# Kernel optimization log

Measured on AMD Instinct MI355X. Metric: run time of the kernel, lower is better.

## Reference

```python
import jax, jax.numpy as jnp
import numpy as np

INPUT_SIZE = 768
HIDDEN = [512, 256, 128]
LATENT = 32
NUM_LEVELS = 3
CODEBOOK_SIZE = 256
BATCH = 131072


def _init_linear(key, d_in, d_out):
    kw, kb = jax.random.split(key)
    lim = 1.0 / np.sqrt(d_in)
    W = jax.random.uniform(kw, (d_in, d_out), jnp.float32, -lim, lim)
    b = jax.random.uniform(kb, (d_out,), jnp.float32, -lim, lim)
    return W, b


def setup_inputs() -> dict:
    key = jax.random.key(0)
    keys = jax.random.split(key, 16)
    inp = {"x": jax.random.normal(keys[0], (BATCH, INPUT_SIZE), jnp.float32)}
    enc_dims = [INPUT_SIZE] + HIDDEN + [LATENT]          # 768->512->256->128->32
    dec_dims = [LATENT] + HIDDEN[::-1] + [INPUT_SIZE]     # 32->128->256->512->768
    for i in range(4):
        W, b = _init_linear(keys[1 + i], enc_dims[i], enc_dims[i + 1])
        inp[f"enc_W{i}"], inp[f"enc_b{i}"] = W, b
        W, b = _init_linear(keys[6 + i], dec_dims[i], dec_dims[i + 1])
        inp[f"dec_W{i}"], inp[f"dec_b{i}"] = W, b
    inp["codebooks"] = jax.random.normal(keys[12], (NUM_LEVELS, CODEBOOK_SIZE, LATENT), jnp.float32)
    return inp


def _mlp(x, Ws, bs):
    # Linear -> ReLU (-> Dropout p=0, identity) between layers, final layer linear.
    n = len(Ws)
    for i in range(n):
        x = x @ Ws[i] + bs[i]
        if i < n - 1:
            x = jax.nn.relu(x)
    return x


def _quantize(z, codebooks):
    # Residual vector quantization over NUM_LEVELS codebooks.
    L, K, D = codebooks.shape
    r = z
    idxs, rs, es = [], [], []
    for l in range(L):
        c = codebooks[l]                                  # [K, D]
        # squared-distance argmin (same argmin as cdist)
        d = jnp.sum(r * r, axis=-1, keepdims=True) - 2.0 * (r @ c.T) + jnp.sum(c * c, axis=-1)
        idx = jnp.argmin(d, axis=-1)                      # [B]
        e = c[idx]                                        # [B, D] gather
        idxs.append(idx)
        rs.append(r)
        es.append(e)
        r = r - e
    quantized = jnp.stack(idxs, axis=1)                   # [B, L] int codes
    r_stack = jnp.stack(rs, axis=1)                       # [B, L, D] residual inputs per level
    e_stack = jnp.stack(es, axis=1)                       # [B, L, D] selected embeddings
    sum_e = jnp.sum(e_stack, axis=1)                      # [B, D]
    # straight-through estimator
    z_hat = z + jax.lax.stop_gradient(sum_e - z)
    counts = jnp.sum(jax.nn.one_hot(quantized, K, dtype=jnp.float32), axis=0)  # [L, K] usage
    return quantized, r_stack, e_stack, z_hat, counts


def reference(x,
              enc_W0, enc_b0, enc_W1, enc_b1, enc_W2, enc_b2, enc_W3, enc_b3,
              dec_W0, dec_b0, dec_W1, dec_b1, dec_W2, dec_b2, dec_W3, dec_b3,
              codebooks):
    encoded = _mlp(x, [enc_W0, enc_W1, enc_W2, enc_W3], [enc_b0, enc_b1, enc_b2, enc_b3])
    quantized, r, e, z_hat, counts = _quantize(encoded, codebooks)
    decoded = _mlp(z_hat, [dec_W0, dec_W1, dec_W2, dec_W3], [dec_b0, dec_b1, dec_b2, dec_b3])
    return decoded, r, e, counts, quantized
```

## Files before the change

kernel.cpp:

```cpp
#include <hip/hip_runtime.h>
#include <hip/hip_bf16.h>
#include <cfloat>

#define B_TOTAL 131072
#define IN_DIM  768
#define NLEV    3
#define KCODE   256

typedef unsigned short u16;
typedef unsigned int   u32;
typedef __attribute__((ext_vector_type(8))) short bf16x8;
typedef __attribute__((ext_vector_type(4))) float f32x4;

#define GLOAD_LDS(g, l)                                                        \
    __builtin_amdgcn_global_load_lds(                                          \
        (const __attribute__((address_space(1))) u32*)(g),                     \
        (__attribute__((address_space(3))) u32*)(l), 16, 0, 0)

__device__ __forceinline__ u16 f2bf(float x) {
    union { __hip_bfloat16 h; u16 u; } c;
    c.h = __float2bfloat16(x);
    return c.u;
}
__device__ __forceinline__ float bf2f(u32 lo16) {
    union { u32 v; float f; } c;
    c.v = lo16 << 16;
    return c.f;
}
__device__ __forceinline__ u32 pack2(float a, float b) {
    return (u32)f2bf(a) | ((u32)f2bf(b) << 16);
}

template<int K, int N, bool AF32, bool RELU, bool OUTF32>
__global__ __launch_bounds__(256)
void gemm_mfma(const void* __restrict__ A_, const u16* __restrict__ Wt,
               const float* __restrict__ bias, void* __restrict__ C_)
{
    constexpr int NK  = K / 32;
    constexpr int NCB = N / 128;
    __shared__ u16 As[2][4096];
    __shared__ u16 Bs[2][4096];

    const int tid  = threadIdx.x;
    const int lane = tid & 63;
    const int wid  = tid >> 6;
    const int wrow = wid >> 1, wcol = wid & 1;

    const u32 nwg  = gridDim.x;
    const u32 orig = blockIdx.x;
    const u32 xcd = orig & 7u, q8 = nwg >> 3, r8 = nwg & 7u;
    const u32 wg = (xcd < r8 ? xcd * (q8 + 1) : r8 * (q8 + 1) + (xcd - r8) * q8)
                 + (orig >> 3);
    const int col0 = (int)(wg % NCB) * 128;
    const int row0 = (int)(wg / NCB) * 128;

    const u16*   Ab = (const u16*)A_;
    const float* Af = (const float*)A_;

    f32x4 acc[4][4];
    #pragma unroll
    for (int i = 0; i < 4; ++i)
        #pragma unroll
        for (int j = 0; j < 4; ++j) acc[i][j] = (f32x4){0.f, 0.f, 0.f, 0.f};

    auto stage_gld = [&](u16* dst, const u16* src ) {
        #pragma unroll
        for (int i = 0; i < 2; ++i) {
            const u32 o   = (u32)(i * 4096 + wid * 1024 + lane * 16);
            const u32 row = o >> 6;
            const u32 cb  = o & 63u;
            const u32 cbs = cb ^ ((row & 3u) << 4);
            const char* g = (const char*)(src + (size_t)row * K) + cbs;
            u16* l = dst + (i * 2048 + wid * 512);
            GLOAD_LDS(g, l);
        }
    };

    float4 fa[4];
    auto loadA_f32 = [&](int kt) {
        const int row = tid >> 1;
        const int ce0 = (tid & 1) * 16;
        const float* s = &Af[(size_t)(row0 + row) * K + kt * 32 + ce0];
        fa[0] = *(const float4*)(s + 0);
        fa[1] = *(const float4*)(s + 4);
        fa[2] = *(const float4*)(s + 8);
        fa[3] = *(const float4*)(s + 12);
    };
    auto writeA_f32 = [&](int buf) {
        const int row = tid >> 1;
        const int cb0 = (tid & 1) * 32;
        const int sw  = (row & 3) << 4;
        char* lb = (char*)&As[buf][0] + row * 64;
        *(uint4*)(lb + ((cb0 + 0) ^ sw)) = make_uint4(
            pack2(fa[0].x, fa[0].y), pack2(fa[0].z, fa[0].w),
            pack2(fa[1].x, fa[1].y), pack2(fa[1].z, fa[1].w));
        *(uint4*)(lb + ((cb0 + 16) ^ sw)) = make_uint4(
            pack2(fa[2].x, fa[2].y), pack2(fa[2].z, fa[2].w),
            pack2(fa[3].x, fa[3].y), pack2(fa[3].z, fa[3].w));
    };

    auto compute = [&](int buf) {
        const char* Ab8 = (const char*)&As[buf][0];
        const char* Bb8 = (const char*)&Bs[buf][0];
        const int kb = (lane >> 4) * 16;
        bf16x8 af[4], bf[4];
        #pragma unroll
        for (int mf = 0; mf < 4; ++mf) {
            const int r = wrow * 64 + mf * 16 + (lane & 15);
            af[mf] = *(const bf16x8*)(Ab8 + r * 64 + (kb ^ ((r & 3) << 4)));
        }
        #pragma unroll
        for (int nf = 0; nf < 4; ++nf) {
            const int r = wcol * 64 + nf * 16 + (lane & 15);
            bf[nf] = *(const bf16x8*)(Bb8 + r * 64 + (kb ^ ((r & 3) << 4)));
        }
        #pragma unroll
        for (int mf = 0; mf < 4; ++mf)
            #pragma unroll
            for (int nf = 0; nf < 4; ++nf)
                acc[mf][nf] = __builtin_amdgcn_mfma_f32_16x16x32_bf16(
                    af[mf], bf[nf], acc[mf][nf], 0, 0, 0);
    };

    if constexpr (AF32) loadA_f32(0);
    stage_gld(&Bs[0][0], Wt + (size_t)col0 * K);
    if constexpr (AF32) writeA_f32(0);
    else                stage_gld(&As[0][0], Ab + (size_t)row0 * K);
    __syncthreads();

    int cur = 0;
    #pragma unroll 1
    for (int kt = 0; kt < NK; ++kt) {
        const bool pref = (kt + 1 < NK);
        if (pref) {
            if constexpr (AF32) loadA_f32(kt + 1);
            stage_gld(&Bs[cur ^ 1][0], Wt + (size_t)col0 * K + (kt + 1) * 32);
            if constexpr (!AF32)
                stage_gld(&As[cur ^ 1][0], Ab + (size_t)row0 * K + (kt + 1) * 32);
        }
        compute(cur);
        if (pref) { if constexpr (AF32) writeA_f32(cur ^ 1); }
        __syncthreads();
        cur ^= 1;
    }

    #pragma unroll
    for (int nf = 0; nf < 4; ++nf) {
        const int col = col0 + wcol * 64 + nf * 16 + (lane & 15);
        const float bv = bias[col];
        #pragma unroll
        for (int mf = 0; mf < 4; ++mf) {
            const int rbase = row0 + wrow * 64 + mf * 16 + (lane >> 4) * 4;
            #pragma unroll
            for (int r = 0; r < 4; ++r) {
                float o = acc[mf][nf][r] + bv;
                if (RELU) o = fmaxf(o, 0.f);
                if constexpr (OUTF32)
                    ((float*)C_)[(size_t)(rbase + r) * N + col] = o;
                else
                    ((u16*)C_)[(size_t)(rbase + r) * N + col] = f2bf(o);
            }
        }
    }
}

template<int K, int N>
__global__ __launch_bounds__(256)
void wcvt(const float* __restrict__ W, u16* __restrict__ Wt)
{
    const int idx = blockIdx.x * 256 + threadIdx.x;
    const int k = idx / N, n = idx - k * N;
    Wt[(size_t)n * K + k] = f2bf(W[idx]);
}

__global__ __launch_bounds__(256)
void vq_kernel(const u16* __restrict__ h3, const float* __restrict__ eW3,
               const float* __restrict__ eb3, const float* __restrict__ cb,
               float* __restrict__ r_out, float* __restrict__ e_out,
               float* __restrict__ q_out, u16* __restrict__ se_ws,
               u32* __restrict__ ghist, size_t grow_base)
{
    __shared__ float W3[128 * 32];
    __shared__ float ebv[32];
    __shared__ float clds[256 * 36];
    __shared__ float cc2[256];
    __shared__ u32   lh[NLEV * KCODE];

    const int tid = threadIdx.x;
    const size_t lrow = (size_t)blockIdx.x * 256 + tid;
    const size_t grow = grow_base + lrow;

    for (int i = tid; i < 128 * 32; i += 256) W3[i] = eW3[i];
    if (tid < 32) ebv[tid] = eb3[tid];
    for (int i = tid; i < NLEV * KCODE; i += 256) lh[i] = 0;
    __syncthreads();

    float r[32];
    #pragma unroll
    for (int j = 0; j < 32; ++j) r[j] = ebv[j];
    {
        const u32* hrow = (const u32*)h3 + lrow * 64;
        #pragma unroll 2
        for (int k2 = 0; k2 < 64; ++k2) {
            const u32 v = hrow[k2];
            const float x0 = bf2f(v & 0xffffu), x1 = bf2f(v >> 16);
            const float* w0 = &W3[(2 * k2) * 32];
            const float* w1 = &W3[(2 * k2 + 1) * 32];
            #pragma unroll
            for (int j4 = 0; j4 < 8; ++j4) {
                const float4 a = *(const float4*)&w0[4 * j4];
                const float4 b = *(const float4*)&w1[4 * j4];
                r[4*j4+0] = fmaf(x1, b.x, fmaf(x0, a.x, r[4*j4+0]));
                r[4*j4+1] = fmaf(x1, b.y, fmaf(x0, a.y, r[4*j4+1]));
                r[4*j4+2] = fmaf(x1, b.z, fmaf(x0, a.z, r[4*j4+2]));
                r[4*j4+3] = fmaf(x1, b.w, fmaf(x0, a.w, r[4*j4+3]));
            }
        }
    }

    float z0[32];
    #pragma unroll
    for (int j = 0; j < 32; ++j) z0[j] = r[j];

    #pragma unroll 1
    for (int l = 0; l < NLEV; ++l) {
        __syncthreads();
        {
            const float* cl = cb + ((size_t)l * KCODE + tid) * 32;
            float s = 0.f;
            #pragma unroll
            for (int m = 0; m < 8; ++m) {
                const float4 v = *(const float4*)&cl[4 * m];
                *(float4*)&clds[tid * 36 + 4 * m] = v;
                s = fmaf(v.x, v.x, s); s = fmaf(v.y, v.y, s);
                s = fmaf(v.z, v.z, s); s = fmaf(v.w, v.w, s);
            }
            cc2[tid] = -0.5f * s;
        }
        __syncthreads();

        float best = -FLT_MAX;
        int   bidx = 0;
        #pragma unroll 1
        for (int k = 0; k < KCODE; ++k) {
            const float* ck = &clds[k * 36];
            float d0 = 0.f, d1 = 0.f, d2 = 0.f, d3 = 0.f;
            #pragma unroll
            for (int m = 0; m < 8; m += 4) {
                const float4 v0 = *(const float4*)&ck[4 * (m + 0)];
                const float4 v1 = *(const float4*)&ck[4 * (m + 1)];
                const float4 v2 = *(const float4*)&ck[4 * (m + 2)];
                const float4 v3 = *(const float4*)&ck[4 * (m + 3)];
                d0 = fmaf(r[4*m+0],  v0.x, d0); d0 = fmaf(r[4*m+1],  v0.y, d0);
                d0 = fmaf(r[4*m+2],  v0.z, d0); d0 = fmaf(r[4*m+3],  v0.w, d0);
                d1 = fmaf(r[4*m+4],  v1.x, d1); d1 = fmaf(r[4*m+5],  v1.y, d1);
                d1 = fmaf(r[4*m+6],  v1.z, d1); d1 = fmaf(r[4*m+7],  v1.w, d1);
                d2 = fmaf(r[4*m+8],  v2.x, d2); d2 = fmaf(r[4*m+9],  v2.y, d2);
                d2 = fmaf(r[4*m+10], v2.z, d2); d2 = fmaf(r[4*m+11], v2.w, d2);
                d3 = fmaf(r[4*m+12], v3.x, d3); d3 = fmaf(r[4*m+13], v3.y, d3);
                d3 = fmaf(r[4*m+14], v3.z, d3); d3 = fmaf(r[4*m+15], v3.w, d3);
            }
            const float s = ((d0 + d1) + (d2 + d3)) + cc2[k];
            if (s > best) { best = s; bidx = k; }
        }

        const size_t base = (grow * NLEV + l) * 32;
        const float* ce = &clds[bidx * 36];
        #pragma unroll
        for (int m = 0; m < 8; ++m) {
            const float4 ev = *(const float4*)&ce[4 * m];
            *(float4*)&r_out[base + 4 * m] =
                make_float4(r[4*m+0], r[4*m+1], r[4*m+2], r[4*m+3]);
            *(float4*)&e_out[base + 4 * m] = ev;
            r[4*m+0] -= ev.x; r[4*m+1] -= ev.y;
            r[4*m+2] -= ev.z; r[4*m+3] -= ev.w;
        }
        q_out[grow * NLEV + l] = (float)bidx;
        atomicAdd(&lh[l * KCODE + bidx], 1u);
    }

    u32* sed = (u32*)se_ws + lrow * 16;
    #pragma unroll
    for (int m = 0; m < 16; ++m)
        sed[m] = pack2(z0[2*m] - r[2*m], z0[2*m+1] - r[2*m+1]);

    __syncthreads();
    for (int i = tid; i < NLEV * KCODE; i += 256)
        if (lh[i]) atomicAdd(&ghist[i], lh[i]);
}

__global__ void zero_hist(u32* h) {
    if (threadIdx.x < NLEV * KCODE) h[threadIdx.x] = 0;
}
__global__ void counts_fin(const u32* __restrict__ g, float* __restrict__ o) {
    if (threadIdx.x < NLEV * KCODE) o[threadIdx.x] = (float)g[threadIdx.x];
}

__global__ __launch_bounds__(256)
void counts_k(const float* __restrict__ q, float* __restrict__ cnt)
{
    const int l = blockIdx.x >> 8;
    const int k = blockIdx.x & 255;
    const float pat = (float)k;
    int c = 0;
    for (int i = threadIdx.x; i < B_TOTAL; i += 256)
        c += (q[(size_t)i * NLEV + l] == pat) ? 1 : 0;
    __shared__ int red[256];
    red[threadIdx.x] = c;
    __syncthreads();
    for (int s = 128; s > 0; s >>= 1) {
        if (threadIdx.x < s) red[threadIdx.x] += red[threadIdx.x + s];
        __syncthreads();
    }
    if (threadIdx.x == 0)
        cnt[blockIdx.x] = (float)red[0];
}

template<int K, int N, bool RELU, bool AGLOBAL>
static __device__ __forceinline__
void layer16(const float* __restrict__ A, size_t grow0,
             const float* __restrict__ W, const float* __restrict__ bias,
             float* __restrict__ C)
{
    constexpr int QPT = N / 128;
    const int tr = threadIdx.x >> 5;
    const int tc = threadIdx.x & 31;
    float acc[2][QPT * 4];
    #pragma unroll
    for (int i = 0; i < 2; ++i)
        #pragma unroll
        for (int j = 0; j < QPT * 4; ++j) acc[i][j] = 0.f;
    #pragma unroll 2
    for (int k0 = 0; k0 < K; k0 += 4) {
        float4 av[2];
        #pragma unroll
        for (int i = 0; i < 2; ++i) {
            if (AGLOBAL)
                av[i] = *(const float4*)&A[(grow0 + tr * 2 + i) * (size_t)K + k0];
            else
                av[i] = *(const float4*)&A[(tr * 2 + i) * K + k0];
        }
        #pragma unroll
        for (int kk = 0; kk < 4; ++kk) {
            #pragma unroll
            for (int q = 0; q < QPT; ++q) {
                const float4 w4 = *(const float4*)&W[(size_t)(k0 + kk) * N + 4 * (tc + 32 * q)];
                #pragma unroll
                for (int i = 0; i < 2; ++i) {
                    const float a = ((const float*)&av[i])[kk];
                    acc[i][4*q+0] = fmaf(a, w4.x, acc[i][4*q+0]);
                    acc[i][4*q+1] = fmaf(a, w4.y, acc[i][4*q+1]);
                    acc[i][4*q+2] = fmaf(a, w4.z, acc[i][4*q+2]);
                    acc[i][4*q+3] = fmaf(a, w4.w, acc[i][4*q+3]);
                }
            }
        }
    }
    #pragma unroll
    for (int q = 0; q < QPT; ++q) {
        const float4 b4 = *(const float4*)&bias[4 * (tc + 32 * q)];
        #pragma unroll
        for (int i = 0; i < 2; ++i) {
            float4 o;
            o.x = acc[i][4*q+0] + b4.x; o.y = acc[i][4*q+1] + b4.y;
            o.z = acc[i][4*q+2] + b4.z; o.w = acc[i][4*q+3] + b4.w;
            if (RELU) {
                o.x = fmaxf(o.x, 0.f); o.y = fmaxf(o.y, 0.f);
                o.z = fmaxf(o.z, 0.f); o.w = fmaxf(o.w, 0.f);
            }
            *(float4*)&C[(tr * 2 + i) * N + 4 * (tc + 32 * q)] = o;
        }
    }
}

static __device__ __forceinline__
void layer_final16(const float* __restrict__ A, const float* __restrict__ W,
                   const float* __restrict__ bias, float* __restrict__ Cg, size_t grow0)
{
    constexpr int QPT = 6;
    const int tr = threadIdx.x >> 5;
    const int tc = threadIdx.x & 31;
    float acc[2][QPT * 4];
    #pragma unroll
    for (int i = 0; i < 2; ++i)
        #pragma unroll
        for (int j = 0; j < QPT * 4; ++j) acc[i][j] = 0.f;
    #pragma unroll 2
    for (int k0 = 0; k0 < 512; k0 += 4) {
        float4 av[2];
        #pragma unroll
        for (int i = 0; i < 2; ++i)
            av[i] = *(const float4*)&A[(tr * 2 + i) * 512 + k0];
        #pragma unroll
        for (int kk = 0; kk < 4; ++kk) {
            #pragma unroll
            for (int q = 0; q < QPT; ++q) {
                const float4 w4 = *(const float4*)&W[(size_t)(k0 + kk) * 768 + 4 * (tc + 32 * q)];
                #pragma unroll
                for (int i = 0; i < 2; ++i) {
                    const float a = ((const float*)&av[i])[kk];
                    acc[i][4*q+0] = fmaf(a, w4.x, acc[i][4*q+0]);
                    acc[i][4*q+1] = fmaf(a, w4.y, acc[i][4*q+1]);
                    acc[i][4*q+2] = fmaf(a, w4.z, acc[i][4*q+2]);
                    acc[i][4*q+3] = fmaf(a, w4.w, acc[i][4*q+3]);
                }
            }
        }
    }
    #pragma unroll
    for (int q = 0; q < QPT; ++q) {
        const float4 b4 = *(const float4*)&bias[4 * (tc + 32 * q)];
        #pragma unroll
        for (int i = 0; i < 2; ++i) {
            float4 s;
            s.x = acc[i][4*q+0] + b4.x; s.y = acc[i][4*q+1] + b4.y;
            s.z = acc[i][4*q+2] + b4.z; s.w = acc[i][4*q+3] + b4.w;
            *(float4*)&Cg[(grow0 + tr * 2 + i) * (size_t)768 + 4 * (tc + 32 * q)] = s;
        }
    }
}

static __device__ __forceinline__
void layer_narrow16(const float* __restrict__ A, const float* __restrict__ W,
                    const float* __restrict__ bias, float* __restrict__ Z)
{
    const int row = threadIdx.x >> 4;
    const int g   = threadIdx.x & 15;
    float a0 = 0.f, a1 = 0.f;
    #pragma unroll 4
    for (int k0 = 0; k0 < 128; k0 += 4) {
        const float4 av = *(const float4*)&A[row * 128 + k0];
        #pragma unroll
        for (int kk = 0; kk < 4; ++kk) {
            const float2 w2 = *(const float2*)&W[(k0 + kk) * 32 + 2 * g];
            const float a = ((const float*)&av)[kk];
            a0 = fmaf(a, w2.x, a0);
            a1 = fmaf(a, w2.y, a1);
        }
    }
    Z[row * 36 + 2 * g + 0] = a0 + bias[2 * g + 0];
    Z[row * 36 + 2 * g + 1] = a1 + bias[2 * g + 1];
}

__global__ __launch_bounds__(256)
void enc_vq_kernel(const float* __restrict__ x,
                   const float* __restrict__ eW0, const float* __restrict__ eb0,
                   const float* __restrict__ eW1, const float* __restrict__ eb1,
                   const float* __restrict__ eW2, const float* __restrict__ eb2,
                   const float* __restrict__ eW3, const float* __restrict__ eb3,
                   const float* __restrict__ cb,
                   float* __restrict__ r_out, float* __restrict__ e_out,
                   float* __restrict__ q_out)
{
    __shared__ __align__(16) char smem[59648];
    float* h1   = (float*)(smem);
    float* h2   = (float*)(smem + 32768);
    float* h3   = (float*)(smem + 49152);
    float* z    = (float*)(smem + 57344);
    float* clds = (float*)(smem);
    float* cc   = (float*)(smem + 36864);

    const size_t grow0 = (size_t)blockIdx.x * 16;
    layer16<768, 512, true, true >(x,  grow0, eW0, eb0, h1);
    __syncthreads();
    layer16<512, 256, true, false>(h1, 0,     eW1, eb1, h2);
    __syncthreads();
    layer16<256, 128, true, false>(h2, 0,     eW2, eb2, h3);
    __syncthreads();
    layer_narrow16(h3, eW3, eb3, z);

    const int row = threadIdx.x >> 4;
    const int g   = threadIdx.x & 15;
    const size_t grow = grow0 + row;

    #pragma unroll 1
    for (int l = 0; l < NLEV; ++l) {
        __syncthreads();
        {
            const float* cl = cb + (size_t)l * KCODE * 32;
            const int t = threadIdx.x;
            float s = 0.f;
            #pragma unroll
            for (int m = 0; m < 8; ++m) {
                const float4 v = *(const float4*)&cl[t * 32 + 4 * m];
                *(float4*)&clds[t * 36 + 4 * m] = v;
                s = fmaf(v.x, v.x, s); s = fmaf(v.y, v.y, s);
                s = fmaf(v.z, v.z, s); s = fmaf(v.w, v.w, s);
            }
            cc[t] = s;
        }
        __syncthreads();

        float r[32];
        #pragma unroll
        for (int m = 0; m < 8; ++m) {
            const float4 v = *(const float4*)&z[row * 36 + 4 * m];
            r[4*m+0] = v.x; r[4*m+1] = v.y; r[4*m+2] = v.z; r[4*m+3] = v.w;
        }
        float rr = 0.f;
        #pragma unroll
        for (int j = 0; j < 32; ++j) rr = fmaf(r[j], r[j], rr);

        float best = FLT_MAX;
        int   bidx = 0x7fffffff;
        #pragma unroll 1
        for (int t = 0; t < 16; ++t) {
            const int k = g + 16 * t;
            const float* ck = &clds[k * 36];
            float d0 = 0.f, d1 = 0.f, d2 = 0.f, d3 = 0.f;
            #pragma unroll
            for (int m = 0; m < 8; m += 4) {
                const float4 v0 = *(const float4*)&ck[4 * (m + 0)];
                const float4 v1 = *(const float4*)&ck[4 * (m + 1)];
                const float4 v2 = *(const float4*)&ck[4 * (m + 2)];
                const float4 v3 = *(const float4*)&ck[4 * (m + 3)];
                d0 = fmaf(r[4*m+0],  v0.x, d0); d0 = fmaf(r[4*m+1],  v0.y, d0);
                d0 = fmaf(r[4*m+2],  v0.z, d0); d0 = fmaf(r[4*m+3],  v0.w, d0);
                d1 = fmaf(r[4*m+4],  v1.x, d1); d1 = fmaf(r[4*m+5],  v1.y, d1);
                d1 = fmaf(r[4*m+6],  v1.z, d1); d1 = fmaf(r[4*m+7],  v1.w, d1);
                d2 = fmaf(r[4*m+8],  v2.x, d2); d2 = fmaf(r[4*m+9],  v2.y, d2);
                d2 = fmaf(r[4*m+10], v2.z, d2); d2 = fmaf(r[4*m+11], v2.w, d2);
                d3 = fmaf(r[4*m+12], v3.x, d3); d3 = fmaf(r[4*m+13], v3.y, d3);
                d3 = fmaf(r[4*m+14], v3.z, d3); d3 = fmaf(r[4*m+15], v3.w, d3);
            }
            const float dot = (d0 + d1) + (d2 + d3);
            const float d = (rr - 2.f * dot) + cc[k];
            if (d < best || (d == best && k < bidx)) { best = d; bidx = k; }
        }
        #pragma unroll
        for (int off = 1; off < 16; off <<= 1) {
            const float ob = __shfl_xor(best, off);
            const int   oi = __shfl_xor(bidx, off);
            if (ob < best || (ob == best && oi < bidx)) { best = ob; bidx = oi; }
        }

        const float evx = clds[bidx * 36 + 2 * g + 0];
        const float evy = clds[bidx * 36 + 2 * g + 1];
        *(float2*)&r_out[(grow * NLEV + l) * 32 + 2 * g] = make_float2(r[2*g], r[2*g+1]);
        *(float2*)&e_out[(grow * NLEV + l) * 32 + 2 * g] = make_float2(evx, evy);
        if (g == 0) q_out[grow * NLEV + l] = (float)bidx;
        z[row * 36 + 2 * g + 0] = r[2 * g + 0] - evx;
        z[row * 36 + 2 * g + 1] = r[2 * g + 1] - evy;
    }
}

__global__ __launch_bounds__(256)
void dec_kernel(const float* __restrict__ e_in,
                const float* __restrict__ dW0, const float* __restrict__ db0,
                const float* __restrict__ dW1, const float* __restrict__ db1,
                const float* __restrict__ dW2, const float* __restrict__ db2,
                const float* __restrict__ dW3, const float* __restrict__ db3,
                float* __restrict__ dec_out)
{
    __shared__ __align__(16) char smem[59392];
    float* h3 = (float*)(smem);
    float* h2 = (float*)(smem + 32768);
    float* h1 = (float*)(smem + 49152);
    float* se = (float*)(smem + 57344);

    const size_t grow0 = (size_t)blockIdx.x * 16;
    const int row = threadIdx.x >> 4;
    const int g   = threadIdx.x & 15;
    {
        const size_t base = ((grow0 + row) * NLEV) * 32 + 2 * g;
        float s0 = 0.f, s1 = 0.f;
        #pragma unroll
        for (int l = 0; l < NLEV; ++l) {
            const float2 v = *(const float2*)&e_in[base + l * 32];
            s0 += v.x; s1 += v.y;
        }
        se[row * 32 + 2 * g + 0] = s0;
        se[row * 32 + 2 * g + 1] = s1;
    }
    __syncthreads();
    layer16<32,  128, true, false>(se, 0, dW0, db0, h1);
    __syncthreads();
    layer16<128, 256, true, false>(h1, 0, dW1, db1, h2);
    __syncthreads();
    layer16<256, 512, true, false>(h2, 0, dW2, db2, h3);
    __syncthreads();
    layer_final16(h3, dW3, db3, dec_out, grow0);
}

extern "C" void kernel_launch(void* const* d_in, const int* in_sizes, int n_in,
                              void* d_out, int out_size, void* d_ws, size_t ws_size,
                              hipStream_t stream)
{
    (void)in_sizes; (void)n_in; (void)out_size;
    const float* x  = (const float*)d_in[0];
    const float* cb = (const float*)d_in[17];
    const float *eW[4], *eb[4], *dW[4], *db[4];
    for (int i = 0; i < 4; ++i) {
        eW[i] = (const float*)d_in[1 + 4 * i];
        eb[i] = (const float*)d_in[2 + 4 * i];
        dW[i] = (const float*)d_in[3 + 4 * i];
        db[i] = (const float*)d_in[4 + 4 * i];
    }

    float* out = (float*)d_out;
    const size_t OFF_R = (size_t)B_TOTAL * IN_DIM;
    const size_t OFF_E = OFF_R + (size_t)B_TOTAL * NLEV * 32;
    const size_t OFF_C = OFF_E + (size_t)B_TOTAL * NLEV * 32;
    const size_t OFF_Q = OFF_C + (size_t)NLEV * KCODE;

    const size_t WTB = 2236416;
    size_t R = 0;
    for (size_t cand = 131072; cand >= 2048; cand >>= 1)
        if (WTB + cand * 3648 + 4096 <= ws_size) { R = cand; break; }

    if (R && d_ws) {
        u16* Wp   = (u16*)d_ws;
        u16* WtE0 = Wp;
        u16* WtE1 = WtE0 + 393216;
        u16* WtE2 = WtE1 + 131072;
        u16* WtD0 = WtE2 + 32768;
        u16* WtD1 = WtD0 + 4096;
        u16* WtD2 = WtD1 + 32768;
        u16* WtD3 = WtD2 + 131072;
        u16* h1   = WtD3 + 393216;
        u16* h2   = h1 + R * 512;
        u16* h3   = h2 + R * 256;
        u16* se   = h3 + R * 128;
        u16* d1   = se + R * 32;
        u16* d2   = d1 + R * 128;
        u16* d3   = d2 + R * 256;
        u32* ghist = (u32*)(d3 + R * 512);

        wcvt<768, 512><<<dim3((768 * 512) / 256), 256, 0, stream>>>(eW[0], WtE0);
        wcvt<512, 256><<<dim3((512 * 256) / 256), 256, 0, stream>>>(eW[1], WtE1);
        wcvt<256, 128><<<dim3((256 * 128) / 256), 256, 0, stream>>>(eW[2], WtE2);
        wcvt<32,  128><<<dim3((32 * 128) / 256),  256, 0, stream>>>(dW[0], WtD0);
        wcvt<128, 256><<<dim3((128 * 256) / 256), 256, 0, stream>>>(dW[1], WtD1);
        wcvt<256, 512><<<dim3((256 * 512) / 256), 256, 0, stream>>>(dW[2], WtD2);
        wcvt<512, 768><<<dim3((512 * 768) / 256), 256, 0, stream>>>(dW[3], WtD3);
        zero_hist<<<1, 768, 0, stream>>>(ghist);

        const int nch = B_TOTAL / (int)R;
        const int MB = (int)R / 128;
        for (int c = 0; c < nch; ++c) {
            const size_t rb = (size_t)c * R;
            gemm_mfma<768, 512, true,  true,  false><<<dim3(4 * MB), 256, 0, stream>>>(
                x + rb * 768, WtE0, eb[0], h1);
            gemm_mfma<512, 256, false, true,  false><<<dim3(2 * MB), 256, 0, stream>>>(
                h1, WtE1, eb[1], h2);
            gemm_mfma<256, 128, false, true,  false><<<dim3(1 * MB), 256, 0, stream>>>(
                h2, WtE2, eb[2], h3);
            vq_kernel<<<dim3((int)R / 256), 256, 0, stream>>>(
                h3, eW[3], eb[3], cb,
                out + OFF_R, out + OFF_E, out + OFF_Q, se, ghist, rb);
            gemm_mfma<32,  128, false, true,  false><<<dim3(1 * MB), 256, 0, stream>>>(
                se, WtD0, db[0], d1);
            gemm_mfma<128, 256, false, true,  false><<<dim3(2 * MB), 256, 0, stream>>>(
                d1, WtD1, db[1], d2);
            gemm_mfma<256, 512, false, true,  false><<<dim3(4 * MB), 256, 0, stream>>>(
                d2, WtD2, db[2], d3);
            gemm_mfma<512, 768, false, false, true ><<<dim3(6 * MB), 256, 0, stream>>>(
                d3, WtD3, db[3], out + rb * 768);
        }
        counts_fin<<<1, 768, 0, stream>>>(ghist, out + OFF_C);
    } else {
        enc_vq_kernel<<<dim3(B_TOTAL / 16), 256, 0, stream>>>(
            x, eW[0], eb[0], eW[1], eb[1], eW[2], eb[2], eW[3], eb[3], cb,
            out + OFF_R, out + OFF_E, out + OFF_Q);
        counts_k<<<dim3(NLEV * KCODE), 256, 0, stream>>>(out + OFF_Q, out + OFF_C);
        dec_kernel<<<dim3(B_TOTAL / 16), 256, 0, stream>>>(
            out + OFF_E, dW[0], db[0], dW[1], db[1], dW[2], db[2], dW[3], db[3], out);
    }
}
```

Baseline: 950.0 us.

## Triple-buffer bf16 GEMM loads and pre-convert input to bf16

```diff
diff --git a/kernel.cpp b/kernel.cpp
--- a/kernel.cpp
+++ b/kernel.cpp
@@ -38,8 +38,8 @@
 {
     constexpr int NK  = K / 32;
     constexpr int NCB = N / 128;
-    __shared__ u16 As[2][4096];
-    __shared__ u16 Bs[2][4096];
+    __shared__ u16 As[3][4096];
+    __shared__ u16 Bs[3][4096];
 
     const int tid  = threadIdx.x;
     const int lane = tid & 63;
@@ -63,40 +63,19 @@
         #pragma unroll
         for (int j = 0; j < 4; ++j) acc[i][j] = (f32x4){0.f, 0.f, 0.f, 0.f};
 
-    auto stage_gld = [&](u16* dst, const u16* src ) {
+    auto stage_one = [&](u16* dstbase, const u16* src) {
         #pragma unroll
         for (int i = 0; i < 2; ++i) {
             const u32 o   = (u32)(i * 4096 + wid * 1024 + lane * 16);
             const u32 row = o >> 6;
-            const u32 cb  = o & 63u;
-            const u32 cbs = cb ^ ((row & 3u) << 4);
-            const char* g = (const char*)(src + (size_t)row * K) + cbs;
-            u16* l = dst + (i * 2048 + wid * 512);
-            GLOAD_LDS(g, l);
+            const u32 cbs = (o & 63u) ^ ((row & 3u) << 4);
+            GLOAD_LDS((const char*)(src + (size_t)row * K) + cbs,
+                      dstbase + (i * 2048 + wid * 512));
         }
     };
-
-    float4 fa[4];
-    auto loadA_f32 = [&](int kt) {
-        const int row = tid >> 1;
-        const int ce0 = (tid & 1) * 16;
-        const float* s = &Af[(size_t)(row0 + row) * K + kt * 32 + ce0];
-        fa[0] = *(const float4*)(s + 0);
-        fa[1] = *(const float4*)(s + 4);
-        fa[2] = *(const float4*)(s + 8);
-        fa[3] = *(const float4*)(s + 12);
-    };
-    auto writeA_f32 = [&](int buf) {
-        const int row = tid >> 1;
-        const int cb0 = (tid & 1) * 32;
-        const int sw  = (row & 3) << 4;
-        char* lb = (char*)&As[buf][0] + row * 64;
-        *(uint4*)(lb + ((cb0 + 0) ^ sw)) = make_uint4(
-            pack2(fa[0].x, fa[0].y), pack2(fa[0].z, fa[0].w),
-            pack2(fa[1].x, fa[1].y), pack2(fa[1].z, fa[1].w));
-        *(uint4*)(lb + ((cb0 + 16) ^ sw)) = make_uint4(
-            pack2(fa[2].x, fa[2].y), pack2(fa[2].z, fa[2].w),
-            pack2(fa[3].x, fa[3].y), pack2(fa[3].z, fa[3].w));
+    auto stage_tile = [&](int buf, int kt) {
+        stage_one(&Bs[buf][0], Wt + (size_t)col0 * K + kt * 32);
+        stage_one(&As[buf][0], Ab + (size_t)row0 * K + kt * 32);
     };
 
     auto compute = [&](int buf) {
@@ -122,26 +101,62 @@
                     af[mf], bf[nf], acc[mf][nf], 0, 0, 0);
     };
 
-    if constexpr (AF32) loadA_f32(0);
-    stage_gld(&Bs[0][0], Wt + (size_t)col0 * K);
-    if constexpr (AF32) writeA_f32(0);
-    else                stage_gld(&As[0][0], Ab + (size_t)row0 * K);
-    __syncthreads();
-
-    int cur = 0;
-    #pragma unroll 1
-    for (int kt = 0; kt < NK; ++kt) {
-        const bool pref = (kt + 1 < NK);
-        if (pref) {
-            if constexpr (AF32) loadA_f32(kt + 1);
-            stage_gld(&Bs[cur ^ 1][0], Wt + (size_t)col0 * K + (kt + 1) * 32);
-            if constexpr (!AF32)
-                stage_gld(&As[cur ^ 1][0], Ab + (size_t)row0 * K + (kt + 1) * 32);
-        }
-        compute(cur);
-        if (pref) { if constexpr (AF32) writeA_f32(cur ^ 1); }
+    if constexpr (AF32) {
+        float4 fa[4];
+        auto loadA = [&](int kt) {
+            const int row = tid >> 1;
+            const int ce0 = (tid & 1) * 16;
+            const float* s = &Af[(size_t)(row0 + row) * K + kt * 32 + ce0];
+            fa[0] = *(const float4*)(s + 0);
+            fa[1] = *(const float4*)(s + 4);
+            fa[2] = *(const float4*)(s + 8);
+            fa[3] = *(const float4*)(s + 12);
+        };
+        auto writeA = [&](int buf) {
+            const int row = tid >> 1;
+            const int cb0 = (tid & 1) * 32;
+            const int sw  = (row & 3) << 4;
+            char* lb = (char*)&As[buf][0] + row * 64;
+            *(uint4*)(lb + ((cb0 + 0) ^ sw)) = make_uint4(
+                pack2(fa[0].x, fa[0].y), pack2(fa[0].z, fa[0].w),
+                pack2(fa[1].x, fa[1].y), pack2(fa[1].z, fa[1].w));
+            *(uint4*)(lb + ((cb0 + 16) ^ sw)) = make_uint4(
+                pack2(fa[2].x, fa[2].y), pack2(fa[2].z, fa[2].w),
+                pack2(fa[3].x, fa[3].y), pack2(fa[3].z, fa[3].w));
+        };
+        loadA(0);
+        stage_one(&Bs[0][0], Wt + (size_t)col0 * K);
+        writeA(0);
         __syncthreads();
-        cur ^= 1;
+        int cur = 0;
+        #pragma unroll 1
+        for (int kt = 0; kt < NK; ++kt) {
+            const bool pref = (kt + 1 < NK);
+            if (pref) {
+                loadA(kt + 1);
+                stage_one(&Bs[cur ^ 1][0], Wt + (size_t)col0 * K + (kt + 1) * 32);
+            }
+            compute(cur);
+            if (pref) writeA(cur ^ 1);
+            __syncthreads();
+            cur ^= 1;
+        }
+    } else {
+        stage_tile(0, 0);
+        if (NK > 1) stage_tile(1, 1);
+        int cb_ = 0, sb_ = 2;
+        #pragma unroll 1
+        for (int kt = 0; kt < NK; ++kt) {
+            if (kt == NK - 1) asm volatile("s_waitcnt vmcnt(0)");
+            else              asm volatile("s_waitcnt vmcnt(4)");
+            __builtin_amdgcn_sched_barrier(0);
+            __builtin_amdgcn_s_barrier();
+            __builtin_amdgcn_sched_barrier(0);
+            if (kt + 2 < NK) stage_tile(sb_, kt + 2);
+            compute(cb_);
+            cb_ = (cb_ == 2) ? 0 : cb_ + 1;
+            sb_ = (sb_ == 2) ? 0 : sb_ + 1;
+        }
     }
 
     #pragma unroll
@@ -171,6 +186,20 @@
     const int idx = blockIdx.x * 256 + threadIdx.x;
     const int k = idx / N, n = idx - k * N;
     Wt[(size_t)n * K + k] = f2bf(W[idx]);
+}
+
+__global__ __launch_bounds__(256)
+void xcvt(const float* __restrict__ x, u16* __restrict__ xb)
+{
+    const size_t n8 = (size_t)B_TOTAL * IN_DIM / 8;
+    const size_t stride = (size_t)gridDim.x * 256;
+    for (size_t i = (size_t)blockIdx.x * 256 + threadIdx.x; i < n8; i += stride) {
+        const float4 a = *(const float4*)&x[i * 8 + 0];
+        const float4 b = *(const float4*)&x[i * 8 + 4];
+        *(uint4*)&xb[i * 8] = make_uint4(
+            pack2(a.x, a.y), pack2(a.z, a.w),
+            pack2(b.x, b.y), pack2(b.z, b.w));
+    }
 }
 
 __global__ __launch_bounds__(256)
@@ -604,9 +633,14 @@
     const size_t OFF_Q = OFF_C + (size_t)NLEV * KCODE;
 
     const size_t WTB = 2236416;
+    const size_t XBB = (size_t)B_TOTAL * IN_DIM * 2;
     size_t R = 0;
+    bool usexb = false;
     for (size_t cand = 131072; cand >= 2048; cand >>= 1)
-        if (WTB + cand * 3648 + 4096 <= ws_size) { R = cand; break; }
+        if (WTB + XBB + cand * 3648 + 4096 <= ws_size) { R = cand; usexb = true; break; }
+    if (!R)
+        for (size_t cand = 131072; cand >= 2048; cand >>= 1)
+            if (WTB + cand * 3648 + 4096 <= ws_size) { R = cand; break; }
 
     if (R && d_ws) {
         u16* Wp   = (u16*)d_ws;
@@ -617,7 +651,10 @@
         u16* WtD1 = WtD0 + 4096;
         u16* WtD2 = WtD1 + 32768;
         u16* WtD3 = WtD2 + 131072;
-        u16* h1   = WtD3 + 393216;
+        u16* Wend = WtD3 + 393216;
+        u16* xb   = Wend;
+        u16* bufs = usexb ? xb + (size_t)B_TOTAL * IN_DIM : Wend;
+        u16* h1   = bufs;
         u16* h2   = h1 + R * 512;
         u16* h3   = h2 + R * 256;
         u16* se   = h3 + R * 128;
@@ -634,13 +671,19 @@
         wcvt<256, 512><<<dim3((256 * 512) / 256), 256, 0, stream>>>(dW[2], WtD2);
         wcvt<512, 768><<<dim3((512 * 768) / 256), 256, 0, stream>>>(dW[3], WtD3);
         zero_hist<<<1, 768, 0, stream>>>(ghist);
+        if (usexb)
+            xcvt<<<dim3(4096), 256, 0, stream>>>(x, xb);
 
         const int nch = B_TOTAL / (int)R;
         const int MB = (int)R / 128;
         for (int c = 0; c < nch; ++c) {
             const size_t rb = (size_t)c * R;
-            gemm_mfma<768, 512, true,  true,  false><<<dim3(4 * MB), 256, 0, stream>>>(
-                x + rb * 768, WtE0, eb[0], h1);
+            if (usexb)
+                gemm_mfma<768, 512, false, true, false><<<dim3(4 * MB), 256, 0, stream>>>(
+                    xb + rb * 768, WtE0, eb[0], h1);
+            else
+                gemm_mfma<768, 512, true,  true, false><<<dim3(4 * MB), 256, 0, stream>>>(
+                    x + rb * 768, WtE0, eb[0], h1);
             gemm_mfma<512, 256, false, true,  false><<<dim3(2 * MB), 256, 0, stream>>>(
                 h1, WtE1, eb[1], h2);
             gemm_mfma<256, 128, false, true,  false><<<dim3(1 * MB), 256, 0, stream>>>(
```

Result: faster. 891.6 us (-6.1%).
